# Kernel optimization log

Measured on AMD Instinct MI355X. Metric: run time of the kernel, lower is better.

The kernel has to match this reference:

```python
import jax, jax.numpy as jnp
import numpy as np

EPS = 1e-12  # F.normalize eps


def _sage(x, k, w_l, b_l, w_r):
    # Faithful to the source's edge_index bug: directed edges i->j (i<j) among
    # global nodes 0..k-1 only (duplicated batch_size times, which leaves the
    # mean unchanged). agg[j] = mean_{i<j} x[i] for j<k; 0 for j>=k (PyG
    # scatter-mean yields 0 for nodes with no in-edges).
    xk = x[:k]                                    # [k, d_in]
    csum = jnp.cumsum(xk, axis=0)                 # [k, d_in]
    prev = jnp.concatenate([jnp.zeros_like(xk[:1]), csum[:-1]], axis=0)
    cnt = jnp.arange(k, dtype=x.dtype)[:, None]   # node j has j in-neighbors
    agg_k = prev / jnp.maximum(cnt, 1.0)          # [k, d_in]
    agg = jnp.zeros_like(x).at[:k].set(agg_k)     # [N, d_in]
    # PyG SAGEConv: out = lin_l(aggr) + lin_r(x); bias lives in lin_l
    out = agg @ w_l.T + b_l + x @ w_r.T           # [N, d_out]
    nrm = jnp.linalg.norm(out, axis=-1, keepdims=True)
    return out / jnp.maximum(nrm, EPS)


def setup_inputs() -> dict:
    key = jax.random.key(0)
    B, K = 32, 1024
    P, I, R = 1024, 128, 256  # problem_size, intermediate_size, rnn_size
    ks = jax.random.split(key, 13)
    dims = [(P, I), (I, 2 * I), (2 * I, I), (I, R)]
    inp = {"flow_matrix": jax.random.normal(ks[0], (B, K, K), dtype=jnp.float32)}
    for li, (din, dout) in enumerate(dims, start=1):
        s = 1.0 / np.sqrt(din)
        inp[f"w_l{li}"] = jax.random.uniform(ks[3 * li - 2], (dout, din), jnp.float32, -s, s)
        inp[f"b_l{li}"] = jax.random.uniform(ks[3 * li - 1], (dout,), jnp.float32, -s, s)
        inp[f"w_r{li}"] = jax.random.uniform(ks[3 * li], (dout, din), jnp.float32, -s, s)
    return inp


def reference(flow_matrix, w_l1, b_l1, w_r1, w_l2, b_l2, w_r2,
              w_l3, b_l3, w_r3, w_l4, b_l4, w_r4):
    B, K, P = flow_matrix.shape
    x = flow_matrix.reshape(-1, P)               # [B*K, P]
    x = _sage(x, K, w_l1, b_l1, w_r1)
    x = _sage(x, K, w_l2, b_l2, w_r2)
    x = _sage(x, K, w_l3, b_l3, w_r3)
    x = _sage(x, K, w_l4, b_l4, w_r4)
    x = jax.nn.relu(x)
    return (x.reshape(B, K, -1), 1)
```

## Files before the change

kernel.cpp:

```cpp
#include <hip/hip_runtime.h>
#include <math.h>


typedef __attribute__((ext_vector_type(8))) short short8;
typedef __attribute__((ext_vector_type(4))) float f32x4;

constexpr int NROWS = 32768;
constexpr int KROWS = 1024;

static __device__ __forceinline__ unsigned short f2bf(float f) {
    unsigned int u = __float_as_uint(f);
    return (unsigned short)((u + 0x7fffu + ((u >> 16) & 1u)) >> 16);
}

template<int ROWS>
struct RegsBF {
    short8 v[ROWS / 32];
    __device__ __forceinline__ void load(const unsigned short* src, int ld,
                                         int r0, int k0, int t) {
#pragma unroll
        for (int j = 0; j < ROWS / 32; ++j) {
            int idx = j * 256 + t; int r = idx >> 3, f = idx & 7;
            v[j] = *reinterpret_cast<const short8*>(
                src + (size_t)(r0 + r) * ld + k0 + f * 8);
        }
    }
    __device__ __forceinline__ void store(unsigned short* buf, int t) {
#pragma unroll
        for (int j = 0; j < ROWS / 32; ++j) {
            int idx = j * 256 + t; int r = idx >> 3, f = idx & 7;
            int off = (r * 128 + f * 16) ^ ((r & 7) << 4);
            *reinterpret_cast<short8*>((char*)buf + off) = v[j];
        }
    }
};

template<int ROWS>
struct RegsF32 {
    float4 v[ROWS / 16];
    __device__ __forceinline__ void load(const float* src, int ld,
                                         int r0, int k0, int t) {
#pragma unroll
        for (int j = 0; j < ROWS / 32; ++j) {
            int idx = j * 256 + t; int r = idx >> 3, f = idx & 7;
            const float* p = src + (size_t)(r0 + r) * ld + k0 + f * 8;
            v[2 * j]     = *reinterpret_cast<const float4*>(p);
            v[2 * j + 1] = *reinterpret_cast<const float4*>(p + 4);
        }
    }
    __device__ __forceinline__ void store(unsigned short* buf, int t) {
#pragma unroll
        for (int j = 0; j < ROWS / 32; ++j) {
            int idx = j * 256 + t; int r = idx >> 3, f = idx & 7;
            float4 a = v[2 * j], b = v[2 * j + 1];
            short8 s;
            s[0] = (short)f2bf(a.x); s[1] = (short)f2bf(a.y);
            s[2] = (short)f2bf(a.z); s[3] = (short)f2bf(a.w);
            s[4] = (short)f2bf(b.x); s[5] = (short)f2bf(b.y);
            s[6] = (short)f2bf(b.z); s[7] = (short)f2bf(b.w);
            int off = (r * 128 + f * 16) ^ ((r & 7) << 4);
            *reinterpret_cast<short8*>((char*)buf + off) = s;
        }
    }
};

template<int BM, int WM, int WN, int FM>
__device__ __forceinline__ void mfma_tile(const unsigned short* Abuf,
    const unsigned short* Bbuf, f32x4 (&acc)[FM][4], int wr_, int wc, int lane)
{
#pragma unroll
    for (int kk = 0; kk < 2; ++kk) {
        short8 a[FM], b[4];
#pragma unroll
        for (int fi = 0; fi < FM; ++fi) {
            const int rA = wr_ * (BM / WM) + fi * 16 + (lane & 15);
            const int off = (rA * 128 + kk * 64 + (lane >> 4) * 16) ^ ((rA & 7) << 4);
            a[fi] = *reinterpret_cast<const short8*>((const char*)Abuf + off);
        }
#pragma unroll
        for (int fj = 0; fj < 4; ++fj) {
            const int rB = wc * 64 + fj * 16 + (lane & 15);
            const int off = (rB * 128 + kk * 64 + (lane >> 4) * 16) ^ ((rB & 7) << 4);
            b[fj] = *reinterpret_cast<const short8*>((const char*)Bbuf + off);
        }
#pragma unroll
        for (int fi = 0; fi < FM; ++fi)
#pragma unroll
            for (int fj = 0; fj < 4; ++fj)
                acc[fi][fj] = __builtin_amdgcn_mfma_f32_16x16x32_bf16(
                    a[fi], b[fj], acc[fi][fj], 0, 0, 0);
    }
}

template<int DIN, int DOUT, bool AFP32, bool BFP32>
__device__ __forceinline__ void proj_dbuf(const void* __restrict__ Xv,
    const void* __restrict__ Wv, unsigned short* __restrict__ YT,
    float* __restrict__ Tg,
    int i0, int t,
    unsigned short* Ab0, unsigned short* Ab1,
    unsigned short* Bb0, unsigned short* Bb1, float* Tred)
{
    constexpr int WN = DOUT / 64, WM = 4 / WN, FM = DOUT / 128, NT = DIN / 64;
    const int wv = t >> 6, lane = t & 63, wr_ = wv / WN, wc = wv % WN;
    f32x4 acc[FM][4];
#pragma unroll
    for (int fi = 0; fi < FM; ++fi)
#pragma unroll
        for (int fj = 0; fj < 4; ++fj) acc[fi][fj] = (f32x4){0.f, 0.f, 0.f, 0.f};

    RegsF32<32>  arf; RegsBF<32>  arb;
    RegsF32<DOUT> brf; RegsBF<DOUT> brb;
    if (AFP32) arf.load((const float*)Xv, DIN, i0, 0, t);
    else       arb.load((const unsigned short*)Xv, DIN, i0, 0, t);
    if (BFP32) brf.load((const float*)Wv, DIN, 0, 0, t);
    else       brb.load((const unsigned short*)Wv, DIN, 0, 0, t);
    if (AFP32) arf.store(Ab0, t); else arb.store(Ab0, t);
    if (BFP32) brf.store(Bb0, t); else brb.store(Bb0, t);
    if (NT > 1) {
        if (AFP32) arf.load((const float*)Xv, DIN, i0, 64, t);
        else       arb.load((const unsigned short*)Xv, DIN, i0, 64, t);
        if (BFP32) brf.load((const float*)Wv, DIN, 0, 64, t);
        else       brb.load((const unsigned short*)Wv, DIN, 0, 64, t);
    }
    __syncthreads();

    for (int kt = 0; kt < NT; ++kt) {
        const unsigned short* Ac = (kt & 1) ? Ab1 : Ab0;
        const unsigned short* Bc = (kt & 1) ? Bb1 : Bb0;
        mfma_tile<32, WM, WN, FM>(Ac, Bc, acc, wr_, wc, lane);
        if (kt + 1 < NT) {
            unsigned short* An = (kt & 1) ? Ab0 : Ab1;
            unsigned short* Bn = (kt & 1) ? Bb0 : Bb1;
            if (AFP32) arf.store(An, t); else arb.store(An, t);
            if (BFP32) brf.store(Bn, t); else brb.store(Bn, t);
            if (kt + 2 < NT) {
                const int kn = (kt + 2) * 64;
                if (AFP32) arf.load((const float*)Xv, DIN, i0, kn, t);
                else       arb.load((const unsigned short*)Xv, DIN, i0, kn, t);
                if (BFP32) brf.load((const float*)Wv, DIN, 0, kn, t);
                else       brb.load((const unsigned short*)Wv, DIN, 0, kn, t);
            }
        }
        __syncthreads();
    }
#pragma unroll
    for (int fi = 0; fi < FM; ++fi)
#pragma unroll
        for (int fj = 0; fj < 4; ++fj) {
            const int rl0 = wr_ * (32 / WM) + fi * 16 + ((lane >> 4) << 2);
            const int cl  = wc * 64 + fj * 16 + (lane & 15);
            ushort4 y;
            y.x = f2bf(acc[fi][fj][0]); y.y = f2bf(acc[fi][fj][1]);
            y.z = f2bf(acc[fi][fj][2]); y.w = f2bf(acc[fi][fj][3]);
            *reinterpret_cast<ushort4*>(YT + (size_t)cl * KROWS + i0 + rl0) = y;
        }
    {
        float v[4];
#pragma unroll
        for (int fj = 0; fj < 4; ++fj) {
            float s = 0.f;
#pragma unroll
            for (int fi = 0; fi < FM; ++fi)
#pragma unroll
                for (int reg = 0; reg < 4; ++reg) s += acc[fi][fj][reg];
            s += __shfl_xor(s, 16);
            s += __shfl_xor(s, 32);
            v[fj] = s;
        }
        if (lane < 16) {
#pragma unroll
            for (int fj = 0; fj < 4; ++fj)
                Tred[wr_ * DOUT + wc * 64 + fj * 16 + lane] = v[fj];
        }
        __syncthreads();
        if (t < DOUT) {
            float s = Tred[t];
            if constexpr (WM == 2) s += Tred[DOUT + t];
            Tg[t] = s;
        }
    }
}

__global__ __launch_bounds__(256, 2)
void prep_kernel(const float* __restrict__ flow, const float* __restrict__ wl1,
                 const float* __restrict__ wr1, const float* __restrict__ wl2,
                 const float* __restrict__ wr2, const float* __restrict__ wl3,
                 const float* __restrict__ wr3, const float* __restrict__ wl4,
                 const float* __restrict__ wr4,
                 unsigned short* __restrict__ wbf,
                 unsigned short* __restrict__ YT1, float* __restrict__ T1,
                 float* __restrict__ outscalar)
{
    __shared__ unsigned short Ab0[32 * 64], Ab1[32 * 64];
    __shared__ unsigned short Bb0[128 * 64], Bb1[128 * 64];
    __shared__ float Tred[256];
    const int t = threadIdx.x, bid = blockIdx.x;
    if (bid >= 32) {
        if (bid == 32 && t == 0) outscalar[0] = 1.0f;
        int g = (bid - 32) * 1024 + t * 4;
        const float* src; int off;
        if      (g < 131072) { src = wr1; off = g; }
        else if (g < 163840) { src = wl2; off = g - 131072; }
        else if (g < 196608) { src = wr2; off = g - 163840; }
        else if (g < 229376) { src = wl3; off = g - 196608; }
        else if (g < 262144) { src = wr3; off = g - 229376; }
        else if (g < 294912) { src = wl4; off = g - 262144; }
        else                 { src = wr4; off = g - 294912; }
        float4 v = *reinterpret_cast<const float4*>(src + off);
        ushort4 o4;
        o4.x = f2bf(v.x); o4.y = f2bf(v.y); o4.z = f2bf(v.z); o4.w = f2bf(v.w);
        *reinterpret_cast<ushort4*>(wbf + g) = o4;
        return;
    }
    proj_dbuf<1024, 128, true, true>(flow, wl1, YT1, T1 + bid * 128,
                                     bid * 32, t, Ab0, Ab1, Bb0, Bb1, Tred);
}

template<int DIN, int DOUT>
__global__ __launch_bounds__(256, 2)
void proj_kernel(const unsigned short* __restrict__ X,
                 const unsigned short* __restrict__ W,
                 unsigned short* __restrict__ YT, float* __restrict__ T)
{
    __shared__ unsigned short Ab0[32 * 64], Ab1[32 * 64];
    __shared__ unsigned short Bb0[DOUT * 64], Bb1[DOUT * 64];
    __shared__ float Tred[256];
    proj_dbuf<DIN, DOUT, false, false>(X, W, YT, T + blockIdx.x * DOUT,
                                       blockIdx.x * 32, threadIdx.x,
                                       Ab0, Ab1, Bb0, Bb1, Tred);
}

template<int DOUT, int BM, int WM, int WN, int MODE, bool AFP32, int MINW>
__global__ __launch_bounds__(256, MINW)
void mfma_gemm(const void* __restrict__ Xv,
               const unsigned short* __restrict__ W,
               const float* __restrict__ bias,
               const unsigned short* __restrict__ YT,
               const float* __restrict__ Tbuf,
               float* __restrict__ outf,
               unsigned short* __restrict__ outb,
               int din)
{
    constexpr int BN = WN * 64;
    static_assert(BN == DOUT, "block must own full output rows");
    constexpr int FM = BM / (WM * 16);
    __shared__ unsigned short Abuf[BM * 64];
    __shared__ unsigned short Bbuf[BN * 64];
    __shared__ float ssred[WN * BM];

    const int t = threadIdx.x, wvid = t >> 6, lane = t & 63;
    const int wr_ = wvid / WN, wc = wvid % WN;
    const int i0 = blockIdx.x * BM;
    const int nt = din >> 6;
    const bool hasagg = (i0 < KROWS);

    f32x4 agg[FM][4];
#pragma unroll
    for (int fi = 0; fi < FM; ++fi)
#pragma unroll
        for (int fj = 0; fj < 4; ++fj) agg[fi][fj] = (f32x4){0.f, 0.f, 0.f, 0.f};

    float Pv[4] = {0.f, 0.f, 0.f, 0.f};
    if (hasagg) {
        const int m = i0 >> 5;
        const int colb = wc * 64 + (lane & 15);
        float Pa[4] = {0.f, 0.f, 0.f, 0.f};
        int mp = 0;
        for (; mp + 1 < m; mp += 2) {
            const float* T0 = Tbuf + (size_t)mp * DOUT + colb;
            const float* T1 = T0 + DOUT;
#pragma unroll
            for (int fj = 0; fj < 4; ++fj) {
                Pv[fj] += T0[fj * 16];
                Pa[fj] += T1[fj * 16];
            }
        }
        if (mp < m) {
            const float* T0 = Tbuf + (size_t)mp * DOUT + colb;
#pragma unroll
            for (int fj = 0; fj < 4; ++fj) Pv[fj] += T0[fj * 16];
        }
#pragma unroll
        for (int fj = 0; fj < 4; ++fj) Pv[fj] += Pa[fj];

        const int base = i0 & ~63;
        RegsBF<BN> sb;
        sb.load(YT, KROWS, 0, base, t);
        sb.store(Bbuf, t);
        __syncthreads();
#pragma unroll
        for (int kk = 0; kk < 2; ++kk) {
            const int jb = base + kk * 32 + ((lane >> 4) << 3);
            short8 a[FM], b[4];
#pragma unroll
            for (int fi = 0; fi < FM; ++fi) {
                const int irow = i0 + wr_ * (BM / WM) + fi * 16 + (lane & 15);
#pragma unroll
                for (int e = 0; e < 8; ++e)
                    a[fi][e] = (short)((jb + e >= i0 && jb + e < irow) ? 0x3F80 : 0);
            }
#pragma unroll
            for (int fj = 0; fj < 4; ++fj) {
                const int rB = wc * 64 + fj * 16 + (lane & 15);
                const int off = (rB * 128 + kk * 64 + (lane >> 4) * 16) ^ ((rB & 7) << 4);
                b[fj] = *reinterpret_cast<const short8*>((const char*)Bbuf + off);
            }
#pragma unroll
            for (int fi = 0; fi < FM; ++fi)
#pragma unroll
                for (int fj = 0; fj < 4; ++fj)
                    agg[fi][fj] = __builtin_amdgcn_mfma_f32_16x16x32_bf16(
                        a[fi], b[fj], agg[fi][fj], 0, 0, 0);
        }
#pragma unroll
        for (int fi = 0; fi < FM; ++fi)
#pragma unroll
            for (int reg = 0; reg < 4; ++reg) {
                const int i_abs = i0 + wr_ * (BM / WM) + fi * 16 + ((lane >> 4) << 2) + reg;
                const float inv = 1.0f / (float)(i_abs > 1 ? i_abs : 1);
#pragma unroll
                for (int fj = 0; fj < 4; ++fj)
                    agg[fi][fj][reg] = (agg[fi][fj][reg] + Pv[fj]) * inv;
            }
        __syncthreads();
    }

    f32x4 acc[FM][4];
#pragma unroll
    for (int fi = 0; fi < FM; ++fi)
#pragma unroll
        for (int fj = 0; fj < 4; ++fj) acc[fi][fj] = (f32x4){0.f, 0.f, 0.f, 0.f};

    RegsBF<BN> brg;
    RegsF32<BM> arf;
    RegsBF<BM> arb;
    if (AFP32) arf.load((const float*)Xv, din, i0, 0, t);
    else       arb.load((const unsigned short*)Xv, din, i0, 0, t);
    brg.load(W, din, 0, 0, t);

    for (int kt = 0; kt < nt; ++kt) {
        if (kt) __syncthreads();
        if (AFP32) arf.store(Abuf, t); else arb.store(Abuf, t);
        brg.store(Bbuf, t);
        __syncthreads();
        if (kt + 1 < nt) {
            int kn = (kt + 1) * 64;
            if (AFP32) arf.load((const float*)Xv, din, i0, kn, t);
            else       arb.load((const unsigned short*)Xv, din, i0, kn, t);
            brg.load(W, din, 0, kn, t);
        }
        mfma_tile<BM, WM, WN, FM>(Abuf, Bbuf, acc, wr_, wc, lane);
    }

    float bb[4];
#pragma unroll
    for (int fj = 0; fj < 4; ++fj) bb[fj] = bias[wc * 64 + fj * 16 + (lane & 15)];

#pragma unroll
    for (int fi = 0; fi < FM; ++fi)
#pragma unroll
        for (int fj = 0; fj < 4; ++fj)
#pragma unroll
            for (int reg = 0; reg < 4; ++reg)
                acc[fi][fj][reg] += bb[fj] + agg[fi][fj][reg];

    float sstot[FM][4];
#pragma unroll
    for (int fi = 0; fi < FM; ++fi)
#pragma unroll
        for (int reg = 0; reg < 4; ++reg) {
            float s = 0.f;
#pragma unroll
            for (int fj = 0; fj < 4; ++fj) {
                float v = acc[fi][fj][reg];
                s += v * v;
            }
#pragma unroll
            for (int m2 = 8; m2 >= 1; m2 >>= 1) s += __shfl_xor(s, m2);
            if ((lane & 15) == 0) {
                int rl = wr_ * (BM / WM) + fi * 16 + ((lane >> 4) << 2) + reg;
                ssred[wc * BM + rl] = s;
            }
        }
    __syncthreads();
#pragma unroll
    for (int fi = 0; fi < FM; ++fi)
#pragma unroll
        for (int reg = 0; reg < 4; ++reg) {
            int rl = wr_ * (BM / WM) + fi * 16 + ((lane >> 4) << 2) + reg;
            float s = 0.f;
#pragma unroll
            for (int c = 0; c < WN; ++c) s += ssred[c * BM + rl];
            sstot[fi][reg] = 1.0f / fmaxf(sqrtf(s), 1e-12f);
        }

#pragma unroll
    for (int fi = 0; fi < FM; ++fi)
#pragma unroll
        for (int fj = 0; fj < 4; ++fj)
#pragma unroll
            for (int reg = 0; reg < 4; ++reg) {
                int rl = wr_ * (BM / WM) + fi * 16 + ((lane >> 4) << 2) + reg;
                int cl = wc * 64 + fj * 16 + (lane & 15);
                float v = acc[fi][fj][reg] * sstot[fi][reg];
                if (MODE == 2) {
                    v = fmaxf(v, 0.f);
                    outf[(size_t)(i0 + rl) * DOUT + cl] = v;
                } else {
                    outb[(size_t)(i0 + rl) * DOUT + cl] = f2bf(v);
                }
            }
}

extern "C" void kernel_launch(void* const* d_in, const int* in_sizes, int n_in,
                              void* d_out, int out_size, void* d_ws, size_t ws_size,
                              hipStream_t stream)
{
    const float* flow = (const float*)d_in[0];
    const float* wl1 = (const float*)d_in[1];
    const float* bl1 = (const float*)d_in[2];
    const float* wr1 = (const float*)d_in[3];
    const float* wl2 = (const float*)d_in[4];
    const float* bl2 = (const float*)d_in[5];
    const float* wr2 = (const float*)d_in[6];
    const float* wl3 = (const float*)d_in[7];
    const float* bl3 = (const float*)d_in[8];
    const float* wr3 = (const float*)d_in[9];
    const float* wl4 = (const float*)d_in[10];
    const float* bl4 = (const float*)d_in[11];
    const float* wr4 = (const float*)d_in[12];
    float* out = (float*)d_out;

    char* p = (char*)d_ws;
    unsigned short* wbf = (unsigned short*)p;  p += 1 << 20;
    unsigned short* xA  = (unsigned short*)p;  p += (size_t)NROWS * 128 * 2;
    unsigned short* xB  = (unsigned short*)p;  p += (size_t)NROWS * 256 * 2;
    unsigned short* YT1 = (unsigned short*)p;  p += (size_t)128 * KROWS * 2;
    unsigned short* YT2 = (unsigned short*)p;  p += (size_t)256 * KROWS * 2;
    unsigned short* YT3 = (unsigned short*)p;  p += (size_t)128 * KROWS * 2;
    unsigned short* YT4 = (unsigned short*)p;  p += (size_t)256 * KROWS * 2;
    float* T1 = (float*)p;                     p += (size_t)32 * 128 * 4;
    float* T2 = (float*)p;                     p += (size_t)32 * 256 * 4;
    float* T3 = (float*)p;                     p += (size_t)32 * 128 * 4;
    float* T4 = (float*)p;

    const unsigned short* wr1b = wbf;
    const unsigned short* wl2b = wbf + 131072;
    const unsigned short* wr2b = wbf + 163840;
    const unsigned short* wl3b = wbf + 196608;
    const unsigned short* wr3b = wbf + 229376;
    const unsigned short* wl4b = wbf + 262144;
    const unsigned short* wr4b = wbf + 294912;

    prep_kernel<<<352, 256, 0, stream>>>(flow, wl1, wr1, wl2, wr2, wl3, wr3,
                                         wl4, wr4, wbf, YT1, T1,
                                         out + (size_t)NROWS * 256);
    mfma_gemm<128, 32, 2, 2, 1, true , 4><<<1024, 256, 0, stream>>>(
        flow, wr1b, bl1, YT1, T1, nullptr, xA, 1024);
    proj_kernel<128, 256><<<32, 256, 0, stream>>>(xA, wl2b, YT2, T2);
    mfma_gemm<256, 32, 1, 4, 1, false, 3><<<1024, 256, 0, stream>>>(
        xA, wr2b, bl2, YT2, T2, nullptr, xB, 128);
    proj_kernel<256, 128><<<32, 256, 0, stream>>>(xB, wl3b, YT3, T3);
    mfma_gemm<128, 32, 2, 2, 1, false, 4><<<1024, 256, 0, stream>>>(
        xB, wr3b, bl3, YT3, T3, nullptr, xA, 256);
    proj_kernel<128, 256><<<32, 256, 0, stream>>>(xA, wl4b, YT4, T4);
    mfma_gemm<256, 32, 1, 4, 2, false, 3><<<1024, 256, 0, stream>>>(
        xA, wr4b, bl4, YT4, T4, out, nullptr, 128);
}
```

Measured before the change: 94.54 us.

## Fuse next-layer projection into GEMM epilogue, removing separate proj kernel launches

The 32 hasagg blocks of each layer's GEMM now compute the next layer's left-weight projection on their freshly written bf16 output tile. This produces YT and the partial column sums in place, replacing three standalone 32-block proj_kernel launches. The goal is to remove launch gaps and the serial low-occupancy proj stages between layers. In exchange those blocks take a longer tail, and the fused path uses a single-buffered loop that syncs every k-step. It also relies on the blocks' own global writes being visible after __syncthreads.

After: 90.82 us (median of 2 runs). -3.9%, faster.

```diff
diff --git a/kernel.cpp b/kernel.cpp
--- a/kernel.cpp
+++ b/kernel.cpp
@@ -92,57 +92,42 @@
     }
 }
 
-template<int DIN, int DOUT, bool AFP32, bool BFP32>
-__device__ __forceinline__ void proj_dbuf(const void* __restrict__ Xv,
-    const void* __restrict__ Wv, unsigned short* __restrict__ YT,
-    float* __restrict__ Tg,
-    int i0, int t,
-    unsigned short* Ab0, unsigned short* Ab1,
-    unsigned short* Bb0, unsigned short* Bb1, float* Tred)
-{
-    constexpr int WN = DOUT / 64, WM = 4 / WN, FM = DOUT / 128, NT = DIN / 64;
+template<int DOUT>
+__device__ __forceinline__ void bulk_gemm_bf(const unsigned short* __restrict__ Av,
+    const unsigned short* __restrict__ W, f32x4 (&acc)[DOUT / 128][4],
+    unsigned short* Abuf, unsigned short* Bbuf, int din, int t)
+{
+    constexpr int WN = DOUT / 64, WM = 4 / WN, FM = DOUT / 128;
     const int wv = t >> 6, lane = t & 63, wr_ = wv / WN, wc = wv % WN;
-    f32x4 acc[FM][4];
+    const int nt = din >> 6;
 #pragma unroll
     for (int fi = 0; fi < FM; ++fi)
 #pragma unroll
         for (int fj = 0; fj < 4; ++fj) acc[fi][fj] = (f32x4){0.f, 0.f, 0.f, 0.f};
-
-    RegsF32<32>  arf; RegsBF<32>  arb;
-    RegsF32<DOUT> brf; RegsBF<DOUT> brb;
-    if (AFP32) arf.load((const float*)Xv, DIN, i0, 0, t);
-    else       arb.load((const unsigned short*)Xv, DIN, i0, 0, t);
-    if (BFP32) brf.load((const float*)Wv, DIN, 0, 0, t);
-    else       brb.load((const unsigned short*)Wv, DIN, 0, 0, t);
-    if (AFP32) arf.store(Ab0, t); else arb.store(Ab0, t);
-    if (BFP32) brf.store(Bb0, t); else brb.store(Bb0, t);
-    if (NT > 1) {
-        if (AFP32) arf.load((const float*)Xv, DIN, i0, 64, t);
-        else       arb.load((const unsigned short*)Xv, DIN, i0, 64, t);
-        if (BFP32) brf.load((const float*)Wv, DIN, 0, 64, t);
-        else       brb.load((const unsigned short*)Wv, DIN, 0, 64, t);
-    }
-    __syncthreads();
-
-    for (int kt = 0; kt < NT; ++kt) {
-        const unsigned short* Ac = (kt & 1) ? Ab1 : Ab0;
-        const unsigned short* Bc = (kt & 1) ? Bb1 : Bb0;
-        mfma_tile<32, WM, WN, FM>(Ac, Bc, acc, wr_, wc, lane);
-        if (kt + 1 < NT) {
-            unsigned short* An = (kt & 1) ? Ab0 : Ab1;
-            unsigned short* Bn = (kt & 1) ? Bb0 : Bb1;
-            if (AFP32) arf.store(An, t); else arb.store(An, t);
-            if (BFP32) brf.store(Bn, t); else brb.store(Bn, t);
-            if (kt + 2 < NT) {
-                const int kn = (kt + 2) * 64;
-                if (AFP32) arf.load((const float*)Xv, DIN, i0, kn, t);
-                else       arb.load((const unsigned short*)Xv, DIN, i0, kn, t);
-                if (BFP32) brf.load((const float*)Wv, DIN, 0, kn, t);
-                else       brb.load((const unsigned short*)Wv, DIN, 0, kn, t);
-            }
-        }
+    RegsBF<32> arb; RegsBF<DOUT> brg;
+    arb.load(Av, din, 0, 0, t);
+    brg.load(W, din, 0, 0, t);
+    for (int kt = 0; kt < nt; ++kt) {
+        if (kt) __syncthreads();
+        arb.store(Abuf, t);
+        brg.store(Bbuf, t);
         __syncthreads();
-    }
+        if (kt + 1 < nt) {
+            const int kn = (kt + 1) * 64;
+            arb.load(Av, din, 0, kn, t);
+            brg.load(W, din, 0, kn, t);
+        }
+        mfma_tile<32, WM, WN, FM>(Abuf, Bbuf, acc, wr_, wc, lane);
+    }
+}
+
+template<int DOUT>
+__device__ __forceinline__ void proj_epilogue(const f32x4 (&acc)[DOUT / 128][4],
+    unsigned short* __restrict__ YT, float* __restrict__ Tg, int i0,
+    float* Tred, int t)
+{
+    constexpr int WN = DOUT / 64, WM = 4 / WN, FM = DOUT / 128;
+    const int wv = t >> 6, lane = t & 63, wr_ = wv / WN, wc = wv % WN;
 #pragma unroll
     for (int fi = 0; fi < FM; ++fi)
 #pragma unroll
@@ -154,31 +139,64 @@
             y.z = f2bf(acc[fi][fj][2]); y.w = f2bf(acc[fi][fj][3]);
             *reinterpret_cast<ushort4*>(YT + (size_t)cl * KROWS + i0 + rl0) = y;
         }
-    {
-        float v[4];
-#pragma unroll
-        for (int fj = 0; fj < 4; ++fj) {
-            float s = 0.f;
-#pragma unroll
-            for (int fi = 0; fi < FM; ++fi)
-#pragma unroll
-                for (int reg = 0; reg < 4; ++reg) s += acc[fi][fj][reg];
-            s += __shfl_xor(s, 16);
-            s += __shfl_xor(s, 32);
-            v[fj] = s;
-        }
-        if (lane < 16) {
-#pragma unroll
-            for (int fj = 0; fj < 4; ++fj)
-                Tred[wr_ * DOUT + wc * 64 + fj * 16 + lane] = v[fj];
+    float v[4];
+#pragma unroll
+    for (int fj = 0; fj < 4; ++fj) {
+        float s = 0.f;
+#pragma unroll
+        for (int fi = 0; fi < FM; ++fi)
+#pragma unroll
+            for (int reg = 0; reg < 4; ++reg) s += acc[fi][fj][reg];
+        s += __shfl_xor(s, 16);
+        s += __shfl_xor(s, 32);
+        v[fj] = s;
+    }
+    if (lane < 16) {
+#pragma unroll
+        for (int fj = 0; fj < 4; ++fj)
+            Tred[wr_ * DOUT + wc * 64 + fj * 16 + lane] = v[fj];
+    }
+    __syncthreads();
+    if (t < DOUT) {
+        float s = Tred[t];
+        if constexpr (WM == 2) s += Tred[DOUT + t];
+        Tg[t] = s;
+    }
+}
+
+__device__ __forceinline__ void proj1_dbuf(const float* __restrict__ flow,
+    const float* __restrict__ wl1, unsigned short* __restrict__ YT1,
+    float* __restrict__ Tg, int i0, int t,
+    unsigned short* Ab0, unsigned short* Ab1,
+    unsigned short* Bb0, unsigned short* Bb1, float* Tred)
+{
+    const int wv = t >> 6, lane = t & 63, wr_ = wv >> 1, wc = wv & 1;
+    f32x4 acc[1][4];
+#pragma unroll
+    for (int fj = 0; fj < 4; ++fj) acc[0][fj] = (f32x4){0.f, 0.f, 0.f, 0.f};
+    RegsF32<32> ar; RegsF32<128> br;
+    ar.load(flow, 1024, i0, 0, t);
+    br.load(wl1, 1024, 0, 0, t);
+    ar.store(Ab0, t); br.store(Bb0, t);
+    ar.load(flow, 1024, i0, 64, t);
+    br.load(wl1, 1024, 0, 64, t);
+    __syncthreads();
+    for (int kt = 0; kt < 16; ++kt) {
+        const unsigned short* Ac = (kt & 1) ? Ab1 : Ab0;
+        const unsigned short* Bc = (kt & 1) ? Bb1 : Bb0;
+        mfma_tile<32, 2, 2, 1>(Ac, Bc, acc, wr_, wc, lane);
+        if (kt + 1 < 16) {
+            unsigned short* An = (kt & 1) ? Ab0 : Ab1;
+            unsigned short* Bn = (kt & 1) ? Bb0 : Bb1;
+            ar.store(An, t); br.store(Bn, t);
+            if (kt + 2 < 16) {
+                ar.load(flow, 1024, i0, (kt + 2) * 64, t);
+                br.load(wl1, 1024, 0, (kt + 2) * 64, t);
+            }
         }
         __syncthreads();
-        if (t < DOUT) {
-            float s = Tred[t];
-            if constexpr (WM == 2) s += Tred[DOUT + t];
-            Tg[t] = s;
-        }
-    }
+    }
+    proj_epilogue<128>(acc, YT1, Tg, i0, Tred, t);
 }
 
 __global__ __launch_bounds__(256, 2)
@@ -212,25 +230,11 @@
         *reinterpret_cast<ushort4*>(wbf + g) = o4;
         return;
     }
-    proj_dbuf<1024, 128, true, true>(flow, wl1, YT1, T1 + bid * 128,
-                                     bid * 32, t, Ab0, Ab1, Bb0, Bb1, Tred);
-}
-
-template<int DIN, int DOUT>
-__global__ __launch_bounds__(256, 2)
-void proj_kernel(const unsigned short* __restrict__ X,
-                 const unsigned short* __restrict__ W,
-                 unsigned short* __restrict__ YT, float* __restrict__ T)
-{
-    __shared__ unsigned short Ab0[32 * 64], Ab1[32 * 64];
-    __shared__ unsigned short Bb0[DOUT * 64], Bb1[DOUT * 64];
-    __shared__ float Tred[256];
-    proj_dbuf<DIN, DOUT, false, false>(X, W, YT, T + blockIdx.x * DOUT,
-                                       blockIdx.x * 32, threadIdx.x,
-                                       Ab0, Ab1, Bb0, Bb1, Tred);
-}
-
-template<int DOUT, int BM, int WM, int WN, int MODE, bool AFP32, int MINW>
+    proj1_dbuf(flow, wl1, YT1, T1 + bid * 128, bid * 32, t,
+               Ab0, Ab1, Bb0, Bb1, Tred);
+}
+
+template<int DOUT, int MODE, bool AFP32, int MINW, int DNEXT>
 __global__ __launch_bounds__(256, MINW)
 void mfma_gemm(const void* __restrict__ Xv,
                const unsigned short* __restrict__ W,
@@ -239,14 +243,17 @@
                const float* __restrict__ Tbuf,
                float* __restrict__ outf,
                unsigned short* __restrict__ outb,
-               int din)
-{
-    constexpr int BN = WN * 64;
-    static_assert(BN == DOUT, "block must own full output rows");
-    constexpr int FM = BM / (WM * 16);
+               int din,
+               const unsigned short* __restrict__ Wn,
+               unsigned short* __restrict__ YTn, float* __restrict__ Tn)
+{
+    constexpr int BM = 32, BN = DOUT;
+    constexpr int WN = DOUT / 64, WM = 4 / WN, FM = DOUT / 128;
+    constexpr int BB = (DNEXT > BN ? DNEXT : BN);
     __shared__ unsigned short Abuf[BM * 64];
-    __shared__ unsigned short Bbuf[BN * 64];
+    __shared__ unsigned short Bbuf[BB * 64];
     __shared__ float ssred[WN * BM];
+    __shared__ float Tred[256];
 
     const int t = threadIdx.x, wvid = t >> 6, lane = t & 63;
     const int wr_ = wvid / WN, wc = wvid % WN;
@@ -260,19 +267,18 @@
 #pragma unroll
         for (int fj = 0; fj < 4; ++fj) agg[fi][fj] = (f32x4){0.f, 0.f, 0.f, 0.f};
 
-    float Pv[4] = {0.f, 0.f, 0.f, 0.f};
     if (hasagg) {
         const int m = i0 >> 5;
         const int colb = wc * 64 + (lane & 15);
-        float Pa[4] = {0.f, 0.f, 0.f, 0.f};
+        float Pv[4] = {0.f, 0.f, 0.f, 0.f}, Pa[4] = {0.f, 0.f, 0.f, 0.f};
         int mp = 0;
         for (; mp + 1 < m; mp += 2) {
             const float* T0 = Tbuf + (size_t)mp * DOUT + colb;
-            const float* T1 = T0 + DOUT;
+            const float* T1p = T0 + DOUT;
 #pragma unroll
             for (int fj = 0; fj < 4; ++fj) {
                 Pv[fj] += T0[fj * 16];
-                Pa[fj] += T1[fj * 16];
+                Pa[fj] += T1p[fj * 16];
             }
         }
         if (mp < m) {
@@ -410,6 +416,17 @@
                     outb[(size_t)(i0 + rl) * DOUT + cl] = f2bf(v);
                 }
             }
+
+    if constexpr (DNEXT > 0) {
+        if (hasagg) {
+            __syncthreads();
+            f32x4 acc2[DNEXT / 128][4];
+            bulk_gemm_bf<DNEXT>(outb + (size_t)i0 * DOUT, Wn, acc2,
+                                Abuf, Bbuf, DOUT, t);
+            __syncthreads();
+            proj_epilogue<DNEXT>(acc2, YTn, Tn + (i0 >> 5) * DNEXT, i0, Tred, t);
+        }
+    }
 }
 
 extern "C" void kernel_launch(void* const* d_in, const int* in_sizes, int n_in,
@@ -455,15 +472,12 @@
     prep_kernel<<<352, 256, 0, stream>>>(flow, wl1, wr1, wl2, wr2, wl3, wr3,
                                          wl4, wr4, wbf, YT1, T1,
                                          out + (size_t)NROWS * 256);
-    mfma_gemm<128, 32, 2, 2, 1, true , 4><<<1024, 256, 0, stream>>>(
-        flow, wr1b, bl1, YT1, T1, nullptr, xA, 1024);
-    proj_kernel<128, 256><<<32, 256, 0, stream>>>(xA, wl2b, YT2, T2);
-    mfma_gemm<256, 32, 1, 4, 1, false, 3><<<1024, 256, 0, stream>>>(
-        xA, wr2b, bl2, YT2, T2, nullptr, xB, 128);
-    proj_kernel<256, 128><<<32, 256, 0, stream>>>(xB, wl3b, YT3, T3);
-    mfma_gemm<128, 32, 2, 2, 1, false, 4><<<1024, 256, 0, stream>>>(
-        xB, wr3b, bl3, YT3, T3, nullptr, xA, 256);
-    proj_kernel<128, 256><<<32, 256, 0, stream>>>(xA, wl4b, YT4, T4);
-    mfma_gemm<256, 32, 1, 4, 2, false, 3><<<1024, 256, 0, stream>>>(
-        xA, wr4b, bl4, YT4, T4, out, nullptr, 128);
-}
+    mfma_gemm<128, 1, true , 4, 256><<<1024, 256, 0, stream>>>(
+        flow, wr1b, bl1, YT1, T1, nullptr, xA, 1024, wl2b, YT2, T2);
+    mfma_gemm<256, 1, false, 3, 128><<<1024, 256, 0, stream>>>(
+        xA, wr2b, bl2, YT2, T2, nullptr, xB, 128, wl3b, YT3, T3);
+    mfma_gemm<128, 1, false, 4, 256><<<1024, 256, 0, stream>>>(
+        xB, wr3b, bl3, YT3, T3, nullptr, xA, 256, wl4b, YT4, T4);
+    mfma_gemm<256, 2, false, 3, 0><<<1024, 256, 0, stream>>>(
+        xA, wr4b, bl4, YT4, T4, out, nullptr, 128, nullptr, nullptr, nullptr);
+}
```
